# Kernel tuning notes

Hardware: AMD Instinct MI355X
Metric: run time of the kernel (lower is better)

## Reference

```python
import jax, jax.numpy as jnp
import numpy as np

B, S, D = 1, 2048, 2048      # batch, seq, hidden
E, F, K = 64, 512, 8         # experts, expert ffn dim, top_k


def setup_inputs() -> dict:
    key = jax.random.key(0)
    ks = jax.random.split(key, 7)
    hidden_states = jax.random.normal(ks[0], (B, S, D), jnp.float32)
    gate_w = jax.random.normal(ks[1], (E, D), jnp.float32) * (D ** -0.5)   # router Linear weight
    w_gate = jax.random.normal(ks[2], (E, F, D), jnp.float32) * 0.02       # expert gate_proj
    w_up   = jax.random.normal(ks[3], (E, F, D), jnp.float32) * 0.02       # expert up_proj
    w_down = jax.random.normal(ks[4], (E, D, F), jnp.float32) * 0.02       # expert down_proj
    token_mod  = jax.random.randint(ks[5], (B * S,), -1, 2).astype(jnp.int32)  # {-1,0,1}
    expert_mod = jax.random.randint(ks[6], (E,), -1, 2).astype(jnp.int32)      # {-1,0,1}
    return {"hidden_states": hidden_states, "gate_w": gate_w, "w_gate": w_gate,
            "w_up": w_up, "w_down": w_down, "token_mod": token_mod,
            "expert_mod": expert_mod}


def reference(hidden_states, gate_w, w_gate, w_up, w_down, token_mod, expert_mod):
    bs = B * S
    x = hidden_states.reshape(bs, D)
    # router gate (Linear, no bias): [bs, E]
    logits = x @ gate_w.T
    # modality pre-filtering: mismatch (tok*exp == -1) -> -inf before softmax
    mismatch = (token_mod[:, None] * expert_mod[None, :]) == -1
    logits = jnp.where(mismatch, -jnp.inf, logits)
    probs = jax.nn.softmax(logits, axis=-1)
    rw, sel = jax.lax.top_k(probs, K)                       # [bs,K]
    rw = rw / jnp.sum(rw, axis=-1, keepdims=True)           # renormalize
    # scatter into sparse routing tensor [bs, E]
    sparse = jnp.zeros((bs, E), x.dtype).at[jnp.arange(bs)[:, None], sel].set(rw)
    # expert dispatch (SwiGLU experts), weighted-sum combine
    g = jnp.einsum('td,efd->tef', x, w_gate)                # [bs,E,F]
    u = jnp.einsum('td,efd->tef', x, w_up)
    h = jax.nn.silu(g) * u
    out = jnp.einsum('te,tef,edf->td', sparse, h, w_down)   # [bs,D]
    return out.reshape(B, S, D)
```

## Files before the change

kernel.cpp:

```cpp
#include <hip/hip_runtime.h>
#include <math.h>

#define BS   2048
#define DIM  2048
#define NE   64
#define NF   512
#define TOPK 8

typedef __attribute__((ext_vector_type(8))) short bf16x8;
typedef __attribute__((ext_vector_type(4))) float f32x4;

__device__ __forceinline__ unsigned cvt2(float lo, float hi) {
    unsigned r;
    asm("v_cvt_pk_bf16_f32 %0, %1, %2" : "=v"(r) : "v"(lo), "v"(hi));
    return r;
}
__device__ __forceinline__ unsigned short f2bf(float f) {
    return (unsigned short)(cvt2(f, 0.f) & 0xFFFF);
}

#define SWZ(r, b) (((((r) << 7) + (b)) ^ (((r) & 7) << 4)))

__global__ __launch_bounds__(256) void zero_kernel(float* __restrict__ out, int* __restrict__ count)
{
    const size_t idx = (size_t)blockIdx.x * blockDim.x + threadIdx.x;
    const size_t tot = (size_t)BS * DIM;
    for (size_t i = idx * 4; i < tot; i += (size_t)gridDim.x * blockDim.x * 4) {
        *(float4*)&out[i] = make_float4(0.f, 0.f, 0.f, 0.f);
    }
    if (idx < NE) count[idx] = 0;
}

__global__ __launch_bounds__(256) void router_kernel(
    const float* __restrict__ x, const float* __restrict__ gate_w,
    const int* __restrict__ token_mod, const int* __restrict__ expert_mod,
    int* __restrict__ count, int* __restrict__ list_token, float* __restrict__ list_w)
{
    __shared__ float xs[4 * DIM];
    __shared__ float pr[4][NE];
    const int t0  = blockIdx.x * 4;
    const int tid = threadIdx.x;
    const int lane = tid & 63, wave = tid >> 6;

    float4* xs4 = (float4*)xs;
    const float4* xr = (const float4*)(x + (size_t)t0 * DIM);
    for (int i = tid; i < 4 * (DIM / 4); i += 256) xs4[i] = xr[i];
    __syncthreads();

    for (int j = 0; j < 16; ++j) {
        const int e = wave * 16 + j;
        const float4* gw = (const float4*)(gate_w + (size_t)e * DIM);
        float s0 = 0.f, s1 = 0.f, s2 = 0.f, s3 = 0.f;
        for (int i = lane; i < DIM / 4; i += 64) {
            const float4 g  = gw[i];
            const float4 v0 = xs4[0 * 512 + i];
            const float4 v1 = xs4[1 * 512 + i];
            const float4 v2 = xs4[2 * 512 + i];
            const float4 v3 = xs4[3 * 512 + i];
            s0 += v0.x * g.x + v0.y * g.y + v0.z * g.z + v0.w * g.w;
            s1 += v1.x * g.x + v1.y * g.y + v1.z * g.z + v1.w * g.w;
            s2 += v2.x * g.x + v2.y * g.y + v2.z * g.z + v2.w * g.w;
            s3 += v3.x * g.x + v3.y * g.y + v3.z * g.z + v3.w * g.w;
        }
        #pragma unroll
        for (int off = 32; off > 0; off >>= 1) {
            s0 += __shfl_xor(s0, off, 64);
            s1 += __shfl_xor(s1, off, 64);
            s2 += __shfl_xor(s2, off, 64);
            s3 += __shfl_xor(s3, off, 64);
        }
        if (lane == 0) {
            pr[0][e] = s0; pr[1][e] = s1; pr[2][e] = s2; pr[3][e] = s3;
        }
    }
    __syncthreads();

    {
        const int t  = t0 + wave;
        const int tm = token_mod[t];
        const int em = expert_mod[lane];
        float p = pr[wave][lane];
        if (tm * em == -1) p = -INFINITY;
        float m0 = p;
        #pragma unroll
        for (int off = 32; off > 0; off >>= 1) m0 = fmaxf(m0, __shfl_xor(m0, off, 64));
        p = __expf(p - m0);
        float s8 = 0.f, wsel = 0.f;
        int   esel = 0;
        #pragma unroll
        for (int k = 0; k < TOPK; ++k) {
            float m = p;
            #pragma unroll
            for (int off = 32; off > 0; off >>= 1) m = fmaxf(m, __shfl_xor(m, off, 64));
            const unsigned long long b = __ballot(p == m);
            const int bi = __ffsll((unsigned long long)b) - 1;
            if (lane == bi) p = -1.f;
            if (lane == k) { esel = bi; wsel = m; }
            s8 += m;
        }
        const float inv = 1.f / s8;
        if (lane < TOPK) {
            const int pos = atomicAdd(&count[esel], 1);
            list_token[esel * BS + pos] = t;
            list_w[esel * BS + pos]     = wsel * inv;
        }
    }
}

__global__ void scan_kernel(const int* __restrict__ count, int* __restrict__ offsets)
{
    if (threadIdx.x == 0) {
        int s = 0;
        for (int e = 0; e < NE; ++e) { offsets[e] = s; s += count[e]; }
    }
}

#define GU_X   0
#define GU_G   8192
#define GU_U   16384

#define GU_COMPUTE()                                                                  \
    {                                                                                 \
        _Pragma("unroll")                                                             \
        for (int ks = 0; ks < 2; ++ks) {                                              \
            const int kb = (ks * 32 + (lane >> 4) * 8) * 2;                           \
            bf16x8 a[2], bg[2], bu[2];                                                \
            _Pragma("unroll")                                                         \
            for (int m = 0; m < 2; ++m)                                               \
                a[m] = *(const bf16x8*)&lds[GU_X + SWZ(wr * 32 + m * 16 + (lane & 15), kb)]; \
            _Pragma("unroll")                                                         \
            for (int nn = 0; nn < 2; ++nn) {                                          \
                const int r = wc * 32 + nn * 16 + (lane & 15);                        \
                bg[nn] = *(const bf16x8*)&lds[GU_G + SWZ(r, kb)];                     \
                bu[nn] = *(const bf16x8*)&lds[GU_U + SWZ(r, kb)];                     \
            }                                                                         \
            _Pragma("unroll")                                                         \
            for (int m = 0; m < 2; ++m)                                               \
                _Pragma("unroll")                                                     \
                for (int nn = 0; nn < 2; ++nn) {                                      \
                    accg[m][nn] = __builtin_amdgcn_mfma_f32_16x16x32_bf16(a[m], bg[nn], accg[m][nn], 0, 0, 0); \
                    accu[m][nn] = __builtin_amdgcn_mfma_f32_16x16x32_bf16(a[m], bu[nn], accu[m][nn], 0, 0, 0); \
                }                                                                     \
        }                                                                             \
    }

#define GU_WRITE()                                                                    \
    {                                                                                 \
        _Pragma("unroll")                                                             \
        for (int i = 0; i < 4; ++i) {                                                 \
            const int r = rr + i * 16;                                                \
            *(uint2*)&lds[GU_X + SWZ(r, c4 * 8)] = make_uint2(cvt2(lx[i].x, lx[i].y), cvt2(lx[i].z, lx[i].w)); \
            *(uint2*)&lds[GU_G + SWZ(r, c4 * 8)] = make_uint2(cvt2(lg[i].x, lg[i].y), cvt2(lg[i].z, lg[i].w)); \
            *(uint2*)&lds[GU_U + SWZ(r, c4 * 8)] = make_uint2(cvt2(lu[i].x, lu[i].y), cvt2(lu[i].z, lu[i].w)); \
        }                                                                             \
    }

__global__ __launch_bounds__(256, 3) void gateup_mfma(
    const float* __restrict__ x,
    const float* __restrict__ w_gate, const float* __restrict__ w_up,
    const int* __restrict__ count, const int* __restrict__ offsets,
    const int* __restrict__ list_token, const float* __restrict__ list_w,
    unsigned short* __restrict__ h)
{
    const int e  = blockIdx.z;
    const int n  = count[e];
    const int m0 = blockIdx.y * 64;
    if (m0 >= n) return;
    const int f0 = blockIdx.x * 64;
    const int mc = min(64, n - m0);

    __shared__ char  lds[24576];
    __shared__ int   toks[64];
    __shared__ float rws[64];

    const int tid = threadIdx.x;
    if (tid < 64) {
        const int idx = e * BS + m0 + (tid < mc ? tid : 0);
        toks[tid] = list_token[idx];
        rws[tid]  = (tid < mc) ? list_w[idx] : 0.f;
    }
    __syncthreads();

    const int lane = tid & 63, wave = tid >> 6;
    const int wr = wave >> 1, wc = wave & 1;
    const int rr = tid >> 4;
    const int c4 = tid & 15;

    const float* xrow[4];
    #pragma unroll
    for (int i = 0; i < 4; ++i) xrow[i] = x + (size_t)toks[rr + i * 16] * DIM + c4 * 4;
    const float* grow[4];
    const float* urow[4];
    #pragma unroll
    for (int i = 0; i < 4; ++i) {
        grow[i] = w_gate + (size_t)e * NF * DIM + (size_t)(f0 + rr + i * 16) * DIM + c4 * 4;
        urow[i] = w_up   + (size_t)e * NF * DIM + (size_t)(f0 + rr + i * 16) * DIM + c4 * 4;
    }

    f32x4 accg[2][2] = {};
    f32x4 accu[2][2] = {};
    float4 lx[4], lg[4], lu[4];

    #pragma unroll
    for (int i = 0; i < 4; ++i) {
        lx[i] = *(const float4*)(xrow[i]);
        lg[i] = *(const float4*)(grow[i]);
        lu[i] = *(const float4*)(urow[i]);
    }
    GU_WRITE();
    __syncthreads();

    for (int t = 0; t < DIM / 64 - 1; ++t) {
        const int doff = (t + 1) * 64;
        #pragma unroll
        for (int i = 0; i < 4; ++i) {
            lx[i] = *(const float4*)(xrow[i] + doff);
            lg[i] = *(const float4*)(grow[i] + doff);
            lu[i] = *(const float4*)(urow[i] + doff);
        }
        __builtin_amdgcn_sched_barrier(0);
        GU_COMPUTE();
        __syncthreads();
        GU_WRITE();
        __syncthreads();
    }
    GU_COMPUTE();

    const int base = offsets[e] + m0;
    #pragma unroll
    for (int m = 0; m < 2; ++m) {
        #pragma unroll
        for (int j = 0; j < 4; ++j) {
            const int tl = wr * 32 + m * 16 + (lane >> 4) * 4 + j;
            if (tl < mc) {
                const float w = rws[tl];
                #pragma unroll
                for (int nn = 0; nn < 2; ++nn) {
                    const int fl = f0 + wc * 32 + nn * 16 + (lane & 15);
                    const float g  = accg[m][nn][j];
                    const float u  = accu[m][nn][j];
                    const float hv = w * u * (g / (1.f + __expf(-g)));
                    h[(size_t)(base + tl) * NF + fl] = f2bf(hv);
                }
            }
        }
    }
}

#define DK_H   0
#define DK_W   8192

#define DK_COMPUTE()                                                                  \
    {                                                                                 \
        _Pragma("unroll")                                                             \
        for (int ks = 0; ks < 2; ++ks) {                                              \
            const int kb = (ks * 32 + (lane >> 4) * 8) * 2;                           \
            bf16x8 a[2], b[4];                                                        \
            _Pragma("unroll")                                                         \
            for (int m = 0; m < 2; ++m)                                               \
                a[m] = *(const bf16x8*)&lds[DK_H + SWZ(wr * 32 + m * 16 + (lane & 15), kb)]; \
            _Pragma("unroll")                                                         \
            for (int nn = 0; nn < 4; ++nn)                                            \
                b[nn] = *(const bf16x8*)&lds[DK_W + SWZ(wc * 64 + nn * 16 + (lane & 15), kb)]; \
            _Pragma("unroll")                                                         \
            for (int m = 0; m < 2; ++m)                                               \
                _Pragma("unroll")                                                     \
                for (int nn = 0; nn < 4; ++nn)                                        \
                    acc[m][nn] = __builtin_amdgcn_mfma_f32_16x16x32_bf16(a[m], b[nn], acc[m][nn], 0, 0, 0); \
        }                                                                             \
    }

#define DK_WRITE()                                                                    \
    {                                                                                 \
        _Pragma("unroll")                                                             \
        for (int i = 0; i < 2; ++i)                                                   \
            *(uint4*)&lds[DK_H + SWZ(hr + i * 32, hc * 2)] = lh[i];                   \
        _Pragma("unroll")                                                             \
        for (int i = 0; i < 8; ++i)                                                   \
            *(uint2*)&lds[DK_W + SWZ(rr + i * 16, c4 * 8)] = make_uint2(cvt2(lw[i].x, lw[i].y), cvt2(lw[i].z, lw[i].w)); \
    }

__global__ __launch_bounds__(256, 3) void down_mfma(
    const float* __restrict__ w_down,
    const int* __restrict__ count, const int* __restrict__ offsets,
    const int* __restrict__ list_token,
    const unsigned short* __restrict__ h, float* __restrict__ out)
{
    const int e  = blockIdx.z;
    const int n  = count[e];
    const int m0 = blockIdx.y * 64;
    if (m0 >= n) return;
    const int d0 = blockIdx.x * 128;
    const int mc = min(64, n - m0);

    __shared__ char lds[24576];
    __shared__ int  toks[64];

    const int tid = threadIdx.x;
    if (tid < 64) toks[tid] = list_token[e * BS + m0 + (tid < mc ? tid : 0)];
    __syncthreads();

    const int lane = tid & 63, wave = tid >> 6;
    const int wr = wave >> 1, wc = wave & 1;
    const int rr = tid >> 4;
    const int c4 = tid & 15;
    const int hr = tid >> 3;
    const int hc = (tid & 7) * 8;

    const float* wd  = w_down + (size_t)e * DIM * NF;
    const int   base = offsets[e] + m0;

    const unsigned short* hrow[2];
    #pragma unroll
    for (int i = 0; i < 2; ++i) {
        const int r  = hr + i * 32;
        const int rs = (r < mc ? r : 0);
        hrow[i] = h + (size_t)(base + rs) * NF + hc;
    }
    const float* wrow[8];
    #pragma unroll
    for (int i = 0; i < 8; ++i) wrow[i] = wd + (size_t)(d0 + rr + i * 16) * NF + c4 * 4;

    f32x4 acc[2][4] = {};
    uint4  lh[2];
    float4 lw[8];

    #pragma unroll
    for (int i = 0; i < 2; ++i) lh[i] = *(const uint4*)(hrow[i]);
    #pragma unroll
    for (int i = 0; i < 8; ++i) lw[i] = *(const float4*)(wrow[i]);
    DK_WRITE();
    __syncthreads();

    for (int t = 0; t < NF / 64 - 1; ++t) {
        const int foff = (t + 1) * 64;
        #pragma unroll
        for (int i = 0; i < 2; ++i) lh[i] = *(const uint4*)(hrow[i] + foff);
        #pragma unroll
        for (int i = 0; i < 8; ++i) lw[i] = *(const float4*)(wrow[i] + foff);
        __builtin_amdgcn_sched_barrier(0);
        DK_COMPUTE();
        __syncthreads();
        DK_WRITE();
        __syncthreads();
    }
    DK_COMPUTE();

    #pragma unroll
    for (int m = 0; m < 2; ++m)
        #pragma unroll
        for (int j = 0; j < 4; ++j) {
            const int sl = wr * 32 + m * 16 + (lane >> 4) * 4 + j;
            if (sl < mc) {
                float* orow = out + (size_t)toks[sl] * DIM + d0 + wc * 64 + (lane & 15);
                #pragma unroll
                for (int nn = 0; nn < 4; ++nn)
                    atomicAdd(&orow[nn * 16], acc[m][nn][j]);
            }
        }
}

extern "C" void kernel_launch(void* const* d_in, const int* in_sizes, int n_in,
                              void* d_out, int out_size, void* d_ws, size_t ws_size,
                              hipStream_t stream)
{
    const float* x          = (const float*)d_in[0];
    const float* gate_w     = (const float*)d_in[1];
    const float* w_gate     = (const float*)d_in[2];
    const float* w_up       = (const float*)d_in[3];
    const float* w_down     = (const float*)d_in[4];
    const int*   token_mod  = (const int*)d_in[5];
    const int*   expert_mod = (const int*)d_in[6];
    float* out = (float*)d_out;

    char* ws = (char*)d_ws;
    unsigned short* h  = (unsigned short*)ws;
    int*   count      = (int*)(ws + 16777216);
    int*   offsets    = (int*)(ws + 16777216 + 256);
    int*   list_token = (int*)(ws + 16777216 + 512);
    float* list_w     = (float*)(ws + 16777216 + 512 + (size_t)NE * BS * 4);

    zero_kernel<<<2048, 256, 0, stream>>>(out, count);
    router_kernel<<<BS / 4, 256, 0, stream>>>(x, gate_w, token_mod, expert_mod,
                                              count, list_token, list_w);
    scan_kernel<<<1, 64, 0, stream>>>(count, offsets);

    dim3 g1(NF / 64, BS / 64, NE);
    gateup_mfma<<<g1, 256, 0, stream>>>(x, w_gate, w_up, count, offsets,
                                        list_token, list_w, h);
    dim3 g2(DIM / 128, BS / 64, NE);
    down_mfma<<<g2, 256, 0, stream>>>(w_down, count, offsets, list_token, h, out);
}
```

Measured before the change: 608.5 us.

## Pre-convert activations to bf16 and launch MoE GEMMs over a compact tile worklist

Adds a kernel that converts x to bf16 once, so the gate/up GEMM loads half the activation bytes for each gathered token and skips per-tile conversion. The scan kernel now also builds a compact list of (expert, m-tile) pairs. Both expert GEMMs launch over this list (MAXT=320 rows) instead of a dense E x BS/64 grid, which removes most of the early-exit empty blocks. The cost is one extra pass over x, extra workspace, and a hard cap of 320 tiles that could overflow if routing were very unbalanced.

Measured after the change: 625.9 us. +2.9%, slower.

```diff
diff --git a/kernel.cpp b/kernel.cpp
--- a/kernel.cpp
+++ b/kernel.cpp
@@ -6,6 +6,7 @@
 #define NE   64
 #define NF   512
 #define TOPK 8
+#define MAXT 320
 
 typedef __attribute__((ext_vector_type(8))) short bf16x8;
 typedef __attribute__((ext_vector_type(4))) float f32x4;
@@ -29,6 +30,17 @@
         *(float4*)&out[i] = make_float4(0.f, 0.f, 0.f, 0.f);
     }
     if (idx < NE) count[idx] = 0;
+}
+
+__global__ __launch_bounds__(256) void cvt_x_kernel(const float* __restrict__ x,
+                                                    unsigned short* __restrict__ xb)
+{
+    const int idx = blockIdx.x * 256 + threadIdx.x;
+    const int tot = BS * DIM / 4;
+    for (int i = idx; i < tot; i += gridDim.x * 256) {
+        const float4 v = *(const float4*)&x[i * 4];
+        *(uint2*)&xb[i * 4] = make_uint2(cvt2(v.x, v.y), cvt2(v.z, v.w));
+    }
 }
 
 __global__ __launch_bounds__(256) void router_kernel(
@@ -107,11 +119,17 @@
     }
 }
 
-__global__ void scan_kernel(const int* __restrict__ count, int* __restrict__ offsets)
+__global__ void scan_kernel(const int* __restrict__ count, int* __restrict__ offsets,
+                            int* __restrict__ worklist, int* __restrict__ ntiles)
 {
     if (threadIdx.x == 0) {
-        int s = 0;
-        for (int e = 0; e < NE; ++e) { offsets[e] = s; s += count[e]; }
+        int s = 0, nt = 0;
+        for (int e = 0; e < NE; ++e) {
+            offsets[e] = s;
+            for (int m0 = 0; m0 < count[e]; m0 += 64) worklist[nt++] = (e << 16) | m0;
+            s += count[e];
+        }
+        ntiles[0] = nt;
     }
 }
 
@@ -147,27 +165,30 @@
 #define GU_WRITE()                                                                    \
     {                                                                                 \
         _Pragma("unroll")                                                             \
+        for (int i = 0; i < 2; ++i)                                                   \
+            *(uint4*)&lds[GU_X + SWZ(xr0 + i * 32, xb0 * 16)] = lxx[i];               \
+        _Pragma("unroll")                                                             \
         for (int i = 0; i < 4; ++i) {                                                 \
             const int r = rr + i * 16;                                                \
-            *(uint2*)&lds[GU_X + SWZ(r, c4 * 8)] = make_uint2(cvt2(lx[i].x, lx[i].y), cvt2(lx[i].z, lx[i].w)); \
             *(uint2*)&lds[GU_G + SWZ(r, c4 * 8)] = make_uint2(cvt2(lg[i].x, lg[i].y), cvt2(lg[i].z, lg[i].w)); \
             *(uint2*)&lds[GU_U + SWZ(r, c4 * 8)] = make_uint2(cvt2(lu[i].x, lu[i].y), cvt2(lu[i].z, lu[i].w)); \
         }                                                                             \
     }
 
 __global__ __launch_bounds__(256, 3) void gateup_mfma(
-    const float* __restrict__ x,
+    const unsigned short* __restrict__ xb,
     const float* __restrict__ w_gate, const float* __restrict__ w_up,
     const int* __restrict__ count, const int* __restrict__ offsets,
+    const int* __restrict__ worklist, const int* __restrict__ ntiles,
     const int* __restrict__ list_token, const float* __restrict__ list_w,
     unsigned short* __restrict__ h)
 {
-    const int e  = blockIdx.z;
-    const int n  = count[e];
-    const int m0 = blockIdx.y * 64;
-    if (m0 >= n) return;
+    if ((int)blockIdx.y >= ntiles[0]) return;
+    const int wl = worklist[blockIdx.y];
+    const int e  = wl >> 16;
+    const int m0 = wl & 0xFFFF;
     const int f0 = blockIdx.x * 64;
-    const int mc = min(64, n - m0);
+    const int mc = min(64, count[e] - m0);
 
     __shared__ char  lds[24576];
     __shared__ int   toks[64];
@@ -185,10 +206,13 @@
     const int wr = wave >> 1, wc = wave & 1;
     const int rr = tid >> 4;
     const int c4 = tid & 15;
-
-    const float* xrow[4];
-    #pragma unroll
-    for (int i = 0; i < 4; ++i) xrow[i] = x + (size_t)toks[rr + i * 16] * DIM + c4 * 4;
+    const int xr0 = tid >> 3;
+    const int xb0 = tid & 7;
+
+    const unsigned short* xrow[2];
+    #pragma unroll
+    for (int i = 0; i < 2; ++i)
+        xrow[i] = xb + (size_t)toks[xr0 + i * 32] * DIM + xb0 * 8;
     const float* grow[4];
     const float* urow[4];
     #pragma unroll
@@ -199,11 +223,13 @@
 
     f32x4 accg[2][2] = {};
     f32x4 accu[2][2] = {};
-    float4 lx[4], lg[4], lu[4];
-
+    uint4  lxx[2];
+    float4 lg[4], lu[4];
+
+    #pragma unroll
+    for (int i = 0; i < 2; ++i) lxx[i] = *(const uint4*)(xrow[i]);
     #pragma unroll
     for (int i = 0; i < 4; ++i) {
-        lx[i] = *(const float4*)(xrow[i]);
         lg[i] = *(const float4*)(grow[i]);
         lu[i] = *(const float4*)(urow[i]);
     }
@@ -213,8 +239,9 @@
     for (int t = 0; t < DIM / 64 - 1; ++t) {
         const int doff = (t + 1) * 64;
         #pragma unroll
+        for (int i = 0; i < 2; ++i) lxx[i] = *(const uint4*)(xrow[i] + doff);
+        #pragma unroll
         for (int i = 0; i < 4; ++i) {
-            lx[i] = *(const float4*)(xrow[i] + doff);
             lg[i] = *(const float4*)(grow[i] + doff);
             lu[i] = *(const float4*)(urow[i] + doff);
         }
@@ -283,15 +310,16 @@
 __global__ __launch_bounds__(256, 3) void down_mfma(
     const float* __restrict__ w_down,
     const int* __restrict__ count, const int* __restrict__ offsets,
+    const int* __restrict__ worklist, const int* __restrict__ ntiles,
     const int* __restrict__ list_token,
     const unsigned short* __restrict__ h, float* __restrict__ out)
 {
-    const int e  = blockIdx.z;
-    const int n  = count[e];
-    const int m0 = blockIdx.y * 64;
-    if (m0 >= n) return;
+    if ((int)blockIdx.y >= ntiles[0]) return;
+    const int wl = worklist[blockIdx.y];
+    const int e  = wl >> 16;
+    const int m0 = wl & 0xFFFF;
     const int d0 = blockIdx.x * 128;
-    const int mc = min(64, n - m0);
+    const int mc = min(64, count[e] - m0);
 
     __shared__ char lds[24576];
     __shared__ int  toks[64];
@@ -375,19 +403,24 @@
 
     char* ws = (char*)d_ws;
     unsigned short* h  = (unsigned short*)ws;
-    int*   count      = (int*)(ws + 16777216);
-    int*   offsets    = (int*)(ws + 16777216 + 256);
-    int*   list_token = (int*)(ws + 16777216 + 512);
-    float* list_w     = (float*)(ws + 16777216 + 512 + (size_t)NE * BS * 4);
+    unsigned short* xb = (unsigned short*)(ws + 16777216);
+    int*   count      = (int*)(ws + 25165824);
+    int*   offsets    = (int*)(ws + 25166080);
+    int*   ntiles     = (int*)(ws + 25166336);
+    int*   worklist   = (int*)(ws + 25166592);
+    int*   list_token = (int*)(ws + 25168640);
+    float* list_w     = (float*)(ws + 25692928);
 
     zero_kernel<<<2048, 256, 0, stream>>>(out, count);
+    cvt_x_kernel<<<1024, 256, 0, stream>>>(x, xb);
     router_kernel<<<BS / 4, 256, 0, stream>>>(x, gate_w, token_mod, expert_mod,
                                               count, list_token, list_w);
-    scan_kernel<<<1, 64, 0, stream>>>(count, offsets);
-
-    dim3 g1(NF / 64, BS / 64, NE);
-    gateup_mfma<<<g1, 256, 0, stream>>>(x, w_gate, w_up, count, offsets,
-                                        list_token, list_w, h);
-    dim3 g2(DIM / 128, BS / 64, NE);
-    down_mfma<<<g2, 256, 0, stream>>>(w_down, count, offsets, list_token, h, out);
-}
+    scan_kernel<<<1, 64, 0, stream>>>(count, offsets, worklist, ntiles);
+
+    dim3 g1(NF / 64, MAXT);
+    gateup_mfma<<<g1, 256, 0, stream>>>(xb, w_gate, w_up, count, offsets,
+                                        worklist, ntiles, list_token, list_w, h);
+    dim3 g2(DIM / 128, MAXT);
+    down_mfma<<<g2, 256, 0, stream>>>(w_down, count, offsets, worklist, ntiles,
+                                      list_token, h, out);
+}
```
